# Optimization experiments

Measured on AMD Instinct MI355X. Metric: run time of the kernel, lower is better.

Reference implementation:

```python
import jax, jax.numpy as jnp
import numpy as np
import math

B, S = 2, 2048
DIM_MODEL = 2048
NUM_Q_HEADS = 16
GROUP_SIZE = 4
NUM_KV_HEADS = NUM_Q_HEADS // GROUP_SIZE
DIM_K = 128
RMS_EPS = 1e-6
ROPE_BASE = 10000.0


def setup_inputs() -> dict:
    key = jax.random.key(0)
    ks = jax.random.split(key, 8)
    x = jax.random.normal(ks[0], (B, S, DIM_MODEL), dtype=jnp.float32)
    mask = jnp.tril(jnp.ones((S, S), dtype=bool))  # causal
    # Linear weights stored as [in, out] so y = x @ W (bias=False everywhere)
    sd = 1.0 / math.sqrt(DIM_MODEL)
    Wq = jax.random.uniform(ks[1], (DIM_MODEL, DIM_K * NUM_Q_HEADS), jnp.float32, -sd, sd)
    Wk = jax.random.uniform(ks[2], (DIM_MODEL, DIM_K * NUM_KV_HEADS), jnp.float32, -sd, sd)
    Wv = jax.random.uniform(ks[3], (DIM_MODEL, DIM_K * NUM_KV_HEADS), jnp.float32, -sd, sd)
    sf = 1.0 / math.sqrt(DIM_K * NUM_Q_HEADS)
    Wfc = jax.random.uniform(ks[4], (DIM_K * NUM_Q_HEADS, DIM_MODEL), jnp.float32, -sf, sf)
    q_gamma = jnp.ones((DIM_K,), dtype=jnp.float32)
    k_gamma = jnp.ones((DIM_K,), dtype=jnp.float32)
    return {"x": x, "mask": mask, "Wq": Wq, "Wk": Wk, "Wv": Wv,
            "Wfc": Wfc, "q_gamma": q_gamma, "k_gamma": k_gamma}


def _rope(t):
    # t: [B, H, S, D], rotate-half RoPE
    d = t.shape[-1]
    half = d // 2
    inv_freq = 1.0 / (ROPE_BASE ** (jnp.arange(half, dtype=jnp.float32) / half))
    pos = jnp.arange(t.shape[2], dtype=jnp.float32)
    ang = pos[:, None] * inv_freq[None, :]            # [S, half]
    cos, sin = jnp.cos(ang), jnp.sin(ang)              # [S, half]
    t1, t2 = t[..., :half], t[..., half:]
    return jnp.concatenate([t1 * cos - t2 * sin, t2 * cos + t1 * sin], axis=-1)


def _rmsnorm(t, gamma):
    ms = jnp.mean(t * t, axis=-1, keepdims=True)
    return t * jax.lax.rsqrt(ms + RMS_EPS) * gamma


def reference(x, mask, Wq, Wk, Wv, Wfc, q_gamma, k_gamma):
    b, s, _ = x.shape
    q = (x @ Wq).reshape(b, s, NUM_Q_HEADS, DIM_K).transpose(0, 2, 1, 3)   # [B,Hq,S,D]
    k = (x @ Wk).reshape(b, s, NUM_KV_HEADS, DIM_K).transpose(0, 2, 1, 3)  # [B,Hkv,S,D]
    v = (x @ Wv).reshape(b, s, NUM_KV_HEADS, DIM_K).transpose(0, 2, 1, 3)
    q = _rmsnorm(_rope(q), q_gamma)
    k = _rmsnorm(_rope(k), k_gamma)
    q = q.reshape(b, NUM_KV_HEADS, GROUP_SIZE, s, DIM_K)                    # [B,Hkv,G,S,D]
    scores = jnp.einsum('bhgqd,bhkd->bhgqk', q, k) / math.sqrt(DIM_K)      # [B,Hkv,G,S,S]
    scores = jnp.where(mask, scores, -jnp.inf)
    attn = jax.nn.softmax(scores, axis=-1)  # dropout is identity in eval
    out = jnp.einsum('bhgqk,bhkd->bhgqd', attn, v)                          # [B,Hkv,G,S,D]
    out = out.reshape(b, NUM_Q_HEADS, s, DIM_K).transpose(0, 2, 1, 3)
    out = out.reshape(b, s, NUM_Q_HEADS * DIM_K) @ Wfc                      # [B,S,DM]
    return out
```

## Files before the change

kernel.cpp:

```cpp
#include <hip/hip_runtime.h>
#include <hip/hip_bf16.h>

typedef __attribute__((ext_vector_type(8))) short bf16x8;
typedef __attribute__((ext_vector_type(4))) short bf16x4;
typedef __attribute__((ext_vector_type(4))) float f32x4;

#define S_LEN 2048
#define DMODEL 2048
#define NQH 16
#define NKVH 4
#define DK 128

__device__ __forceinline__ float b2f(short u) {
  union { unsigned int i; float f; } x;
  x.i = ((unsigned int)(unsigned short)u) << 16;
  return x.f;
}
__device__ __forceinline__ short f2b(float f) {
  union { float f; unsigned int i; } x; x.f = f;
  unsigned int r = (x.i + 0x7fffu + ((x.i >> 16) & 1u)) >> 16;
  return (short)r;
}
__device__ __forceinline__ unsigned int cvtpk(float a, float b) {
  unsigned int r;
  asm("v_cvt_pk_bf16_f32 %0, %1, %2" : "=v"(r) : "v"(a), "v"(b));
  return r;
}
__device__ __forceinline__ f32x4 mfma16(bf16x8 a, bf16x8 b, f32x4 c) {
  return __builtin_amdgcn_mfma_f32_16x16x32_bf16(a, b, c, 0, 0, 0);
}
__device__ __forceinline__ void async16(short* lds, const short* g) {
  __builtin_amdgcn_global_load_lds(
      (const __attribute__((address_space(1))) unsigned int*)(const void*)g,
      (__attribute__((address_space(3))) unsigned int*)(void*)lds, 16, 0, 0);
}

__global__ void f32_to_bf16(const float* __restrict__ in, short* __restrict__ out, int n4) {
  int i = blockIdx.x * blockDim.x + threadIdx.x;
  if (i >= n4) return;
  float4 v = ((const float4*)in)[i];
  bf16x4 o;
  o[0] = f2b(v.x); o[1] = f2b(v.y); o[2] = f2b(v.z); o[3] = f2b(v.w);
  ((bf16x4*)out)[i] = o;
}

__global__ void rope_table(float* __restrict__ rt) {
  int i = blockIdx.x * blockDim.x + threadIdx.x;
  int s = i >> 6, d = i & 63;
  float ang = (float)s * __expf((float)d * -0.14391157f);
  float c, sn;
  __sincosf(ang, &sn, &c);
  rt[s * 128 + d] = c;
  rt[s * 128 + 64 + d] = sn;
}

__global__ void transpose_f2b(const float* __restrict__ in, short* __restrict__ out,
                              int R, int C) {
  __shared__ short t[32][33];
  int c0 = blockIdx.x * 32, r0 = blockIdx.y * 32;
  int tx = threadIdx.x, ty = threadIdx.y;
#pragma unroll
  for (int i = 0; i < 32; i += 8)
    t[ty + i][tx] = f2b(in[(size_t)(r0 + ty + i) * C + c0 + tx]);
  __syncthreads();
#pragma unroll
  for (int i = 0; i < 32; i += 8)
    out[(size_t)(c0 + ty + i) * R + r0 + tx] = t[tx][ty + i];
}

__device__ __forceinline__ void stage_tile64(short* Ls, const short* Gb, int ldg,
                                             int w, int lane) {
#pragma unroll
  for (int i = 0; i < 4; ++i) {
    const int r0 = w * 32 + i * 8;
    const int row = r0 + (lane >> 3);
    const int colb = ((lane & 7) * 8) ^ ((row & 7) << 3);
    async16(Ls + r0 * 64, Gb + (size_t)row * ldg + colb);
  }
}

__global__ __launch_bounds__(256) void gemm_qkv(const short* __restrict__ A,
                                                const short* __restrict__ WT,
                                                short* __restrict__ Qr,
                                                short* __restrict__ Kr,
                                                short* __restrict__ Vtr,
                                                const float* __restrict__ qg,
                                                const float* __restrict__ kg,
                                                const float* __restrict__ ropeT) {
  constexpr int CS_LD = 136;
  __shared__ __align__(16) short smem[4 * 128 * 64];

  const int flat = blockIdx.x;
  const int xcd = flat & 7, idx = flat >> 3;
  const int mb = (xcd >> 1) * 8 + (idx & 7);
  const int nb = (xcd & 1) * 12 + (idx >> 3);

  const int tid = threadIdx.x;
  const int lane = tid & 63;
  const int w = tid >> 6;
  const int wm = w >> 1, wn = w & 1;
  const int l15 = lane & 15, lg = lane >> 4;
  const int K = DMODEL;
  constexpr int NSTEP = DMODEL / 64;

  f32x4 acc[4][4] = {};
  const short* Ab = A + (size_t)mb * 128 * K;
  const short* Bb = WT + (size_t)nb * 128 * K;

  stage_tile64(smem, Ab, K, w, lane);
  stage_tile64(smem + 8192, Bb, K, w, lane);
  asm volatile("s_waitcnt vmcnt(0)" ::: "memory");
  __syncthreads();

  for (int t = 0; t < NSTEP; ++t) {
    const int cur = t & 1;
    short* Ac = smem + cur * 16384;
    short* Bc = Ac + 8192;
    if (t + 1 < NSTEP) {
      short* An = smem + (cur ^ 1) * 16384;
      stage_tile64(An, Ab + (t + 1) * 64, K, w, lane);
      stage_tile64(An + 8192, Bb + (t + 1) * 64, K, w, lane);
    }
#pragma unroll
    for (int kk = 0; kk < 2; ++kk) {
      bf16x8 af[4], bfr[4];
#pragma unroll
      for (int mt = 0; mt < 4; ++mt)
        af[mt] = *(const bf16x8*)(Ac + (wm * 64 + mt * 16 + l15) * 64 +
                                  ((kk * 32 + lg * 8) ^ ((l15 & 7) << 3)));
#pragma unroll
      for (int nt = 0; nt < 4; ++nt)
        bfr[nt] = *(const bf16x8*)(Bc + (wn * 64 + nt * 16 + l15) * 64 +
                                   ((kk * 32 + lg * 8) ^ ((l15 & 7) << 3)));
#pragma unroll
      for (int mt = 0; mt < 4; ++mt)
#pragma unroll
        for (int nt = 0; nt < 4; ++nt)
          acc[mt][nt] = mfma16(af[mt], bfr[nt], acc[mt][nt]);
    }
    asm volatile("s_waitcnt vmcnt(0)" ::: "memory");
    __syncthreads();
  }

  short* Cs = smem;
#pragma unroll
  for (int mt = 0; mt < 4; ++mt)
#pragma unroll
    for (int nt = 0; nt < 4; ++nt)
#pragma unroll
      for (int r = 0; r < 4; ++r)
        Cs[(wm * 64 + mt * 16 + lg * 4 + r) * CS_LD + wn * 64 + nt * 16 + l15] =
            f2b(acc[mt][nt][r]);
  __syncthreads();

  const int srow0 = mb * 128;
  const int b = srow0 >> 11;

  if (nb < 20) {
    const bool isQ = nb < 16;
    const int h = isQ ? nb : nb - 16;
    const float* gamma = isQ ? qg : kg;
    const int r = tid >> 1, half = tid & 1;
    const int s = (srow0 + r) & 2047;
    const float* rt = ropeT + (size_t)s * 128;
    float ss = 0.f;
    bf16x8 ov[8];
#pragma unroll
    for (int j = 0; j < 8; ++j) {
      bf16x8 t1v = *(const bf16x8*)(Cs + r * CS_LD + j * 8);
      bf16x8 t2v = *(const bf16x8*)(Cs + r * CS_LD + 64 + j * 8);
      float4 c0 = *(const float4*)(rt + j * 8);
      float4 c1 = *(const float4*)(rt + j * 8 + 4);
      float4 s0 = *(const float4*)(rt + 64 + j * 8);
      float4 s1 = *(const float4*)(rt + 64 + j * 8 + 4);
      float cc[8] = {c0.x, c0.y, c0.z, c0.w, c1.x, c1.y, c1.z, c1.w};
      float sn[8] = {s0.x, s0.y, s0.z, s0.w, s1.x, s1.y, s1.z, s1.w};
#pragma unroll
      for (int i = 0; i < 8; ++i) {
        float t1 = b2f(t1v[i]), t2 = b2f(t2v[i]);
        float o = half ? (t2 * cc[i] + t1 * sn[i]) : (t1 * cc[i] - t2 * sn[i]);
        ss += o * o;
        ov[j][i] = f2b(o);
      }
    }
    ss += __shfl_xor(ss, 1);
    float inv = rsqrtf(ss * (1.0f / 128.0f) + 1e-6f);
    if (isQ) inv *= (0.08838834764831845f * 1.4426950408889634f);
    const int NH = isQ ? NQH : NKVH;
    short* outp = isQ ? Qr : Kr;
    short* ob = outp + ((size_t)(b * NH + h) * S_LEN + s) * DK + half * 64;
#pragma unroll
    for (int j = 0; j < 8; ++j) {
      float4 g0 = *(const float4*)(gamma + half * 64 + j * 8);
      float4 g1 = *(const float4*)(gamma + half * 64 + j * 8 + 4);
      float gg[8] = {g0.x, g0.y, g0.z, g0.w, g1.x, g1.y, g1.z, g1.w};
      bf16x8 vv;
#pragma unroll
      for (int i = 0; i < 8; ++i) vv[i] = f2b(b2f(ov[j][i]) * inv * gg[i]);
      *(bf16x8*)(ob + j * 8) = vv;
    }
  } else {
    const int h = nb - 20;
    const int d = tid & 127;
    const int sh = tid >> 7;
    const int sbase = (srow0 & 2047) + sh * 64;
    short* ob = Vtr + ((size_t)(b * NKVH + h) * DK + d) * S_LEN + sbase;
    for (int i0 = 0; i0 < 64; i0 += 8) {
      bf16x8 v;
#pragma unroll
      for (int j = 0; j < 8; ++j) {
        const int p = i0 + j;
        const int sl = sh * 64 + 16 * (p & 3) + (p >> 2);
        v[j] = Cs[sl * CS_LD + d];
      }
      *(bf16x8*)(ob + i0) = v;
    }
  }
}

__global__ __launch_bounds__(256) void gemm_out(const short* __restrict__ A,
                                                const short* __restrict__ BT,
                                                float* __restrict__ outf) {
  __shared__ __align__(16) short smem[4 * 128 * 64];

  const int flat = blockIdx.x;
  const int xcd = flat & 7, idx = flat >> 3;
  const int mb = (xcd >> 1) * 8 + (idx & 7);
  const int nb = (xcd & 1) * 8 + (idx >> 3);

  const int tid = threadIdx.x;
  const int lane = tid & 63;
  const int w = tid >> 6;
  const int wm = w >> 1, wn = w & 1;
  const int l15 = lane & 15, lg = lane >> 4;
  const int K = NQH * DK, N = DMODEL;
  constexpr int NSTEP = (NQH * DK) / 64;

  f32x4 acc[4][4] = {};
  const short* Ab = A + (size_t)mb * 128 * K;
  const short* Bb = BT + (size_t)nb * 128 * K;

  stage_tile64(smem, Ab, K, w, lane);
  stage_tile64(smem + 8192, Bb, K, w, lane);
  asm volatile("s_waitcnt vmcnt(0)" ::: "memory");
  __syncthreads();

  for (int t = 0; t < NSTEP; ++t) {
    const int cur = t & 1;
    short* Ac = smem + cur * 16384;
    short* Bc = Ac + 8192;
    if (t + 1 < NSTEP) {
      short* An = smem + (cur ^ 1) * 16384;
      stage_tile64(An, Ab + (t + 1) * 64, K, w, lane);
      stage_tile64(An + 8192, Bb + (t + 1) * 64, K, w, lane);
    }
#pragma unroll
    for (int kk = 0; kk < 2; ++kk) {
      bf16x8 af[4], bfr[4];
#pragma unroll
      for (int mt = 0; mt < 4; ++mt)
        af[mt] = *(const bf16x8*)(Ac + (wm * 64 + mt * 16 + l15) * 64 +
                                  ((kk * 32 + lg * 8) ^ ((l15 & 7) << 3)));
#pragma unroll
      for (int nt = 0; nt < 4; ++nt)
        bfr[nt] = *(const bf16x8*)(Bc + (wn * 64 + nt * 16 + l15) * 64 +
                                   ((kk * 32 + lg * 8) ^ ((l15 & 7) << 3)));
#pragma unroll
      for (int mt = 0; mt < 4; ++mt)
#pragma unroll
        for (int nt = 0; nt < 4; ++nt)
          acc[mt][nt] = mfma16(af[mt], bfr[nt], acc[mt][nt]);
    }
    asm volatile("s_waitcnt vmcnt(0)" ::: "memory");
    __syncthreads();
  }

#pragma unroll
  for (int mt = 0; mt < 4; ++mt) {
    const int row = mb * 128 + wm * 64 + mt * 16 + lg * 4;
#pragma unroll
    for (int nt = 0; nt < 4; ++nt) {
      const int col = nb * 128 + wn * 64 + nt * 16 + l15;
#pragma unroll
      for (int r = 0; r < 4; ++r)
        outf[(size_t)(row + r) * N + col] = acc[mt][nt][r];
    }
  }
}

__device__ __forceinline__ void stage_kv(const short* __restrict__ Kb,
                                         const short* __restrict__ Vb, int kb,
                                         short* Ks, short* Vs, int w, int lane) {
#pragma unroll
  for (int i = 0; i < 4; ++i) {
    const int c = 4 * w + i;
    const int krow = c * 4 + (lane >> 4);
    const int kcol = (((lane & 15) * 16) ^ ((krow & 7) << 4)) >> 1;
    async16(Ks + c * 512, Kb + (size_t)(kb + krow) * DK + kcol);
    const int vrow = c * 8 + (lane >> 3);
    const int vcol = (((lane & 7) * 16) ^ ((vrow & 7) << 4)) >> 1;
    async16(Vs + c * 512, Vb + (size_t)vrow * S_LEN + kb + vcol);
  }
}

__device__ __forceinline__ void sm_pv(f32x4* sc, float* lsum, f32x4* acco,
                                      const short* Vc, short* Pw, int q0, bool diag,
                                      int kb, int l15, int lg) {
  if (diag) {
#pragma unroll
    for (int nt = 0; nt < 4; ++nt) {
      const int k = kb + nt * 16 + l15;
#pragma unroll
      for (int r = 0; r < 4; ++r)
        if (k > q0 + lg * 4 + r) sc[nt][r] = -1e30f;
    }
  }
#pragma unroll
  for (int r = 0; r < 4; ++r) {
    const float p0 = exp2f(sc[0][r]);
    const float p1 = exp2f(sc[1][r]);
    const float p2 = exp2f(sc[2][r]);
    const float p3 = exp2f(sc[3][r]);
    lsum[r] += (p0 + p1) + (p2 + p3);
    uint2 dv;
    dv.x = cvtpk(p0, p1);
    dv.y = cvtpk(p2, p3);
    *(uint2*)(Pw + (lg * 4 + r) * 72 + l15 * 4) = dv;
  }
#pragma unroll
  for (int kk = 0; kk < 2; ++kk) {
    bf16x8 ap = *(const bf16x8*)(Pw + l15 * 72 + kk * 32 + lg * 8);
#pragma unroll
    for (int dt = 0; dt < 8; ++dt) {
      const int vrow = dt * 16 + l15;
      bf16x8 bv = *(const bf16x8*)(Vc + vrow * 64 +
                                   (((kk * 64 + lg * 16) ^ ((vrow & 7) << 4)) >> 1));
      acco[dt] = mfma16(ap, bv, acco[dt]);
    }
  }
}

__device__ __forceinline__ void attn_writeout(f32x4* acco, float* lsum,
                                              short* __restrict__ AO, int b, int qh,
                                              int q0, int l15, int lg) {
  float ls[4];
#pragma unroll
  for (int r = 0; r < 4; ++r) {
    float t = lsum[r];
    t += __shfl_xor(t, 1);
    t += __shfl_xor(t, 2);
    t += __shfl_xor(t, 4);
    t += __shfl_xor(t, 8);
    ls[r] = 1.0f / t;
  }
  short* ob = AO + (size_t)(b * S_LEN + q0) * (NQH * DK) + qh * DK;
#pragma unroll
  for (int dt = 0; dt < 8; ++dt)
#pragma unroll
    for (int r = 0; r < 4; ++r)
      ob[(size_t)(lg * 4 + r) * (NQH * DK) + dt * 16 + l15] = f2b(acco[dt][r] * ls[r]);
}

__global__ __launch_bounds__(256, 2) void attn_kernel(const short* __restrict__ Qr,
                                                      const short* __restrict__ Kr,
                                                      const short* __restrict__ Vt,
                                                      short* __restrict__ AO) {
  const int flat = blockIdx.x;
  const int nw = (flat & 7) * 64 + (flat >> 3);
  const int qtA = nw & 15;
  const int bh = nw >> 4;
  const int qtB = 31 - qtA;
  const int b = bh >> 4, qh = bh & 15;
  const int kvh = qh >> 2;
  const short* Qb = Qr + (size_t)bh * S_LEN * DK;
  const short* Kb = Kr + (size_t)(b * NKVH + kvh) * S_LEN * DK;
  const short* Vb = Vt + (size_t)(b * NKVH + kvh) * DK * S_LEN;
  const int tid = threadIdx.x, lane = tid & 63, w = tid >> 6;
  const int l15 = lane & 15, lg = lane >> 4;

  __shared__ __align__(16) short KV[4][64 * 128];
  __shared__ __align__(16) short P[4][16][72];
  short* Pw = &P[w][0][0];

  const int q0A = qtA * 64 + w * 16, q0B = qtB * 64 + w * 16;
  bf16x8 aqA[4], aqB[4];
#pragma unroll
  for (int kk = 0; kk < 4; ++kk) {
    aqA[kk] = *(const bf16x8*)(Qb + (size_t)(q0A + l15) * DK + kk * 32 + lg * 8);
    aqB[kk] = *(const bf16x8*)(Qb + (size_t)(q0B + l15) * DK + kk * 32 + lg * 8);
  }

  f32x4 accoA[8] = {}, accoB[8] = {};
  float lsA[4] = {0.f, 0.f, 0.f, 0.f}, lsB[4] = {0.f, 0.f, 0.f, 0.f};

  short* Kcur = KV[0]; short* Vcur = KV[1];
  short* Knxt = KV[2]; short* Vnxt = KV[3];

  stage_kv(Kb, Vb, 0, Kcur, Vcur, w, lane);
  asm volatile("s_waitcnt vmcnt(0)" ::: "memory");
  __syncthreads();

  for (int kt = 0; kt <= qtB; ++kt) {
    const int kb = kt * 64;
    if (kt < qtB) stage_kv(Kb, Vb, kb + 64, Knxt, Vnxt, w, lane);

    if (kt <= qtA) {
      f32x4 scB[4] = {}, scA[4] = {};
#pragma unroll
      for (int kk = 0; kk < 4; ++kk)
#pragma unroll
        for (int nt = 0; nt < 4; ++nt) {
          const int krow = nt * 16 + l15;
          bf16x8 bk = *(const bf16x8*)(Kcur + krow * 128 +
                                       (((kk * 64 + lg * 16) ^ ((krow & 7) << 4)) >> 1));
          scB[nt] = mfma16(aqB[kk], bk, scB[nt]);
          scA[nt] = mfma16(aqA[kk], bk, scA[nt]);
        }
      sm_pv(scB, lsB, accoB, Vcur, Pw, q0B, false, kb, l15, lg);
      sm_pv(scA, lsA, accoA, Vcur, Pw, q0A, kt == qtA, kb, l15, lg);
    } else {
      f32x4 scB[4] = {};
#pragma unroll
      for (int kk = 0; kk < 4; ++kk)
#pragma unroll
        for (int nt = 0; nt < 4; ++nt) {
          const int krow = nt * 16 + l15;
          bf16x8 bk = *(const bf16x8*)(Kcur + krow * 128 +
                                       (((kk * 64 + lg * 16) ^ ((krow & 7) << 4)) >> 1));
          scB[nt] = mfma16(aqB[kk], bk, scB[nt]);
        }
      sm_pv(scB, lsB, accoB, Vcur, Pw, q0B, kt == qtB, kb, l15, lg);
    }

    asm volatile("s_waitcnt vmcnt(0)" ::: "memory");
    __syncthreads();
    short* t;
    t = Kcur; Kcur = Knxt; Knxt = t;
    t = Vcur; Vcur = Vnxt; Vnxt = t;
  }

  attn_writeout(accoB, lsB, AO, b, qh, q0B, l15, lg);
  attn_writeout(accoA, lsA, AO, b, qh, q0A, l15, lg);
}

extern "C" void kernel_launch(void* const* d_in, const int* in_sizes, int n_in,
                              void* d_out, int out_size, void* d_ws, size_t ws_size,
                              hipStream_t stream) {
  const float* x = (const float*)d_in[0];
  const float* Wq = (const float*)d_in[2];
  const float* Wk = (const float*)d_in[3];
  const float* Wv = (const float*)d_in[4];
  const float* Wfc = (const float*)d_in[5];
  const float* qg = (const float*)d_in[6];
  const float* kg = (const float*)d_in[7];

  short* ws = (short*)d_ws;
  short* xb = ws;
  short* WqkvT = xb + (size_t)4096 * 2048;
  short* WqT = WqkvT;
  short* WkT = WqT + (size_t)2048 * 2048;
  short* WvT = WkT + (size_t)512 * 2048;
  short* WfcT = WvT + (size_t)512 * 2048;
  short* Qr = WfcT + (size_t)2048 * 2048;
  short* Kr = Qr + (size_t)32 * 2048 * 128;
  short* Vt = Kr + (size_t)8 * 2048 * 128;
  float* ropeT = (float*)(Vt + (size_t)8 * 128 * 2048);
  short* AO = xb;

  f32_to_bf16<<<(4096 * 2048 / 4 + 255) / 256, 256, 0, stream>>>(x, xb, 4096 * 2048 / 4);
  rope_table<<<(2048 * 64 + 255) / 256, 256, 0, stream>>>(ropeT);

  dim3 tb(32, 8);
  transpose_f2b<<<dim3(2048 / 32, 2048 / 32), tb, 0, stream>>>(Wq, WqT, 2048, 2048);
  transpose_f2b<<<dim3(512 / 32, 2048 / 32), tb, 0, stream>>>(Wk, WkT, 2048, 512);
  transpose_f2b<<<dim3(512 / 32, 2048 / 32), tb, 0, stream>>>(Wv, WvT, 2048, 512);
  transpose_f2b<<<dim3(2048 / 32, 2048 / 32), tb, 0, stream>>>(Wfc, WfcT, 2048, 2048);

  gemm_qkv<<<768, 256, 0, stream>>>(xb, WqkvT, Qr, Kr, Vt, qg, kg, ropeT);

  attn_kernel<<<512, 256, 0, stream>>>(Qr, Kr, Vt, AO);

  gemm_out<<<512, 256, 0, stream>>>(AO, WfcT, (float*)d_out);
}
```

Baseline: 198.1 us.

## Restructure GEMM mainloop into half-K-step staging with partial vmcnt waits

Replaces the double-buffered 64-wide K-step loop in both projection GEMMs with a shared core. It stages 32-wide K halves into separate LDS slices using a new XOR swizzle, and waits with vmcnt(4) so one half-tile load stays in flight while the other is consumed. The full vmcnt(0) drain per step goes away, and plain s_barrier replaces __syncthreads. This trades more barriers per K-step for finer-grained overlap, and hardcodes K=2048 for both kernels.

```diff
diff --git a/kernel.cpp b/kernel.cpp
--- a/kernel.cpp
+++ b/kernel.cpp
@@ -68,15 +68,89 @@
     out[(size_t)(c0 + ty + i) * R + r0 + tx] = t[tx][ty + i];
 }
 
-__device__ __forceinline__ void stage_tile64(short* Ls, const short* Gb, int ldg,
-                                             int w, int lane) {
-#pragma unroll
-  for (int i = 0; i < 4; ++i) {
-    const int r0 = w * 32 + i * 8;
-    const int row = r0 + (lane >> 3);
-    const int colb = ((lane & 7) * 8) ^ ((row & 7) << 3);
-    async16(Ls + r0 * 64, Gb + (size_t)row * ldg + colb);
-  }
+__device__ __forceinline__ void kcore128(const short* __restrict__ Ab,
+                                         const short* __restrict__ Bb,
+                                         short* sm, f32x4 (&acc)[4][4],
+                                         int w, int lane, int wm, int wn,
+                                         int l15, int lg) {
+  const int K = 2048;
+  const int srow = 32 * w + (lane >> 2);
+  const int colp = (((lane & 3) ^ ((srow >> 1) & 3)) * 8);
+  const short* pA0 = Ab + (size_t)srow * K + colp;
+  const short* pA1 = pA0 + (size_t)16 * K;
+  const short* pB0 = Bb + (size_t)srow * K + colp;
+  const short* pB1 = pB0 + (size_t)16 * K;
+  const int sdst = w * 1024;
+  const int perm = (l15 >> 1) & 3;
+  const int aoff = (wm * 64 + l15) * 32 + ((lg ^ perm) * 8);
+  const int boff = 8192 + (wn * 64 + l15) * 32 + ((lg ^ perm) * 8);
+
+  auto stage = [&](int bufn, int tn, int h) {
+    short* d = sm + bufn * 16384 + h * 4096 + sdst;
+    const int off = tn * 64 + h * 32;
+    async16(d, pA0 + off);
+    async16(d + 512, pA1 + off);
+    async16(d + 8192, pB0 + off);
+    async16(d + 8192 + 512, pB1 + off);
+  };
+  auto half = [&](int bc, int h) {
+    const short* base = sm + bc * 16384 + h * 4096;
+    bf16x8 af[4], bfr[4];
+#pragma unroll
+    for (int mt = 0; mt < 4; ++mt) af[mt] = *(const bf16x8*)(base + aoff + mt * 512);
+#pragma unroll
+    for (int nt = 0; nt < 4; ++nt) bfr[nt] = *(const bf16x8*)(base + boff + nt * 512);
+#pragma unroll
+    for (int mt = 0; mt < 4; ++mt)
+#pragma unroll
+      for (int nt = 0; nt < 4; ++nt)
+        acc[mt][nt] = mfma16(af[mt], bfr[nt], acc[mt][nt]);
+  };
+
+  stage(0, 0, 0);
+  stage(0, 0, 1);
+
+#pragma unroll 1
+  for (int tt = 0; tt < 30; tt += 2) {
+    asm volatile("s_waitcnt vmcnt(4)" ::: "memory");
+    __builtin_amdgcn_s_barrier();
+    asm volatile("" ::: "memory");
+    stage(1, tt + 1, 0);
+    half(0, 0);
+    asm volatile("s_waitcnt vmcnt(4)" ::: "memory");
+    __builtin_amdgcn_s_barrier();
+    asm volatile("" ::: "memory");
+    stage(1, tt + 1, 1);
+    half(0, 1);
+    asm volatile("s_waitcnt vmcnt(4)" ::: "memory");
+    __builtin_amdgcn_s_barrier();
+    asm volatile("" ::: "memory");
+    stage(0, tt + 2, 0);
+    half(1, 0);
+    asm volatile("s_waitcnt vmcnt(4)" ::: "memory");
+    __builtin_amdgcn_s_barrier();
+    asm volatile("" ::: "memory");
+    stage(0, tt + 2, 1);
+    half(1, 1);
+  }
+  asm volatile("s_waitcnt vmcnt(4)" ::: "memory");
+  __builtin_amdgcn_s_barrier();
+  asm volatile("" ::: "memory");
+  stage(1, 31, 0);
+  half(0, 0);
+  asm volatile("s_waitcnt vmcnt(4)" ::: "memory");
+  __builtin_amdgcn_s_barrier();
+  asm volatile("" ::: "memory");
+  stage(1, 31, 1);
+  half(0, 1);
+  asm volatile("s_waitcnt vmcnt(4)" ::: "memory");
+  __builtin_amdgcn_s_barrier();
+  asm volatile("" ::: "memory");
+  half(1, 0);
+  asm volatile("s_waitcnt vmcnt(0)" ::: "memory");
+  __builtin_amdgcn_s_barrier();
+  asm volatile("" ::: "memory");
+  half(1, 1);
 }
 
 __global__ __launch_bounds__(256) void gemm_qkv(const short* __restrict__ A,
@@ -88,7 +162,7 @@
                                                 const float* __restrict__ kg,
                                                 const float* __restrict__ ropeT) {
   constexpr int CS_LD = 136;
-  __shared__ __align__(16) short smem[4 * 128 * 64];
+  __shared__ __align__(16) short smem[32768];
 
   const int flat = blockIdx.x;
   const int xcd = flat & 7, idx = flat >> 3;
@@ -101,47 +175,12 @@
   const int wm = w >> 1, wn = w & 1;
   const int l15 = lane & 15, lg = lane >> 4;
   const int K = DMODEL;
-  constexpr int NSTEP = DMODEL / 64;
 
   f32x4 acc[4][4] = {};
-  const short* Ab = A + (size_t)mb * 128 * K;
-  const short* Bb = WT + (size_t)nb * 128 * K;
-
-  stage_tile64(smem, Ab, K, w, lane);
-  stage_tile64(smem + 8192, Bb, K, w, lane);
-  asm volatile("s_waitcnt vmcnt(0)" ::: "memory");
+  kcore128(A + (size_t)mb * 128 * K, WT + (size_t)nb * 128 * K, smem, acc,
+           w, lane, wm, wn, l15, lg);
+
   __syncthreads();
-
-  for (int t = 0; t < NSTEP; ++t) {
-    const int cur = t & 1;
-    short* Ac = smem + cur * 16384;
-    short* Bc = Ac + 8192;
-    if (t + 1 < NSTEP) {
-      short* An = smem + (cur ^ 1) * 16384;
-      stage_tile64(An, Ab + (t + 1) * 64, K, w, lane);
-      stage_tile64(An + 8192, Bb + (t + 1) * 64, K, w, lane);
-    }
-#pragma unroll
-    for (int kk = 0; kk < 2; ++kk) {
-      bf16x8 af[4], bfr[4];
-#pragma unroll
-      for (int mt = 0; mt < 4; ++mt)
-        af[mt] = *(const bf16x8*)(Ac + (wm * 64 + mt * 16 + l15) * 64 +
-                                  ((kk * 32 + lg * 8) ^ ((l15 & 7) << 3)));
-#pragma unroll
-      for (int nt = 0; nt < 4; ++nt)
-        bfr[nt] = *(const bf16x8*)(Bc + (wn * 64 + nt * 16 + l15) * 64 +
-                                   ((kk * 32 + lg * 8) ^ ((l15 & 7) << 3)));
-#pragma unroll
-      for (int mt = 0; mt < 4; ++mt)
-#pragma unroll
-        for (int nt = 0; nt < 4; ++nt)
-          acc[mt][nt] = mfma16(af[mt], bfr[nt], acc[mt][nt]);
-    }
-    asm volatile("s_waitcnt vmcnt(0)" ::: "memory");
-    __syncthreads();
-  }
-
   short* Cs = smem;
 #pragma unroll
   for (int mt = 0; mt < 4; ++mt)
@@ -221,7 +260,7 @@
 __global__ __launch_bounds__(256) void gemm_out(const short* __restrict__ A,
                                                 const short* __restrict__ BT,
                                                 float* __restrict__ outf) {
-  __shared__ __align__(16) short smem[4 * 128 * 64];
+  __shared__ __align__(16) short smem[32768];
 
   const int flat = blockIdx.x;
   const int xcd = flat & 7, idx = flat >> 3;
@@ -234,46 +273,10 @@
   const int wm = w >> 1, wn = w & 1;
   const int l15 = lane & 15, lg = lane >> 4;
   const int K = NQH * DK, N = DMODEL;
-  constexpr int NSTEP = (NQH * DK) / 64;
 
   f32x4 acc[4][4] = {};
-  const short* Ab = A + (size_t)mb * 128 * K;
-  const short* Bb = BT + (size_t)nb * 128 * K;
-
-  stage_tile64(smem, Ab, K, w, lane);
-  stage_tile64(smem + 8192, Bb, K, w, lane);
-  asm volatile("s_waitcnt vmcnt(0)" ::: "memory");
-  __syncthreads();
-
-  for (int t = 0; t < NSTEP; ++t) {
-    const int cur = t & 1;
-    short* Ac = smem + cur * 16384;
-    short* Bc = Ac + 8192;
-    if (t + 1 < NSTEP) {
-      short* An = smem + (cur ^ 1) * 16384;
-      stage_tile64(An, Ab + (t + 1) * 64, K, w, lane);
-      stage_tile64(An + 8192, Bb + (t + 1) * 64, K, w, lane);
-    }
-#pragma unroll
-    for (int kk = 0; kk < 2; ++kk) {
-      bf16x8 af[4], bfr[4];
-#pragma unroll
-      for (int mt = 0; mt < 4; ++mt)
-        af[mt] = *(const bf16x8*)(Ac + (wm * 64 + mt * 16 + l15) * 64 +
-                                  ((kk * 32 + lg * 8) ^ ((l15 & 7) << 3)));
-#pragma unroll
-      for (int nt = 0; nt < 4; ++nt)
-        bfr[nt] = *(const bf16x8*)(Bc + (wn * 64 + nt * 16 + l15) * 64 +
-                                   ((kk * 32 + lg * 8) ^ ((l15 & 7) << 3)));
-#pragma unroll
-      for (int mt = 0; mt < 4; ++mt)
-#pragma unroll
-        for (int nt = 0; nt < 4; ++nt)
-          acc[mt][nt] = mfma16(af[mt], bfr[nt], acc[mt][nt]);
-    }
-    asm volatile("s_waitcnt vmcnt(0)" ::: "memory");
-    __syncthreads();
-  }
+  kcore128(A + (size_t)mb * 128 * K, BT + (size_t)nb * 128 * K, smem, acc,
+           w, lane, wm, wn, l15, lg);
 
 #pragma unroll
   for (int mt = 0; mt < 4; ++mt) {
```

After: 199.3 us. About the same (+0.6%).

## Rewrite QKV and output GEMMs with 256-row tiles and triple-buffered pipeline

Applied to the files above, without the earlier changes.

Both projection GEMMs move to a shared 512-thread core with 256x256 (QKV) and 256x128 (out) block tiles, a K-step of 32 and three LDS buffers. Loads are issued asynchronously, interleaved with MFMA, and raised with s_setprio so global traffic overlaps compute. The QKV epilogue now runs in two 128-row phases covering two heads per tile. Bigger tiles raise arithmetic intensity and cut block count, but 192 or 256 blocks may leave parts of the 256 CUs idle, and register pressure rises.

```diff
diff --git a/kernel.cpp b/kernel.cpp
--- a/kernel.cpp
+++ b/kernel.cpp
@@ -68,18 +68,102 @@
     out[(size_t)(c0 + ty + i) * R + r0 + tx] = t[tx][ty + i];
 }
 
-__device__ __forceinline__ void stage_tile64(short* Ls, const short* Gb, int ldg,
-                                             int w, int lane) {
-#pragma unroll
-  for (int i = 0; i < 4; ++i) {
-    const int r0 = w * 32 + i * 8;
-    const int row = r0 + (lane >> 3);
-    const int colb = ((lane & 7) * 8) ^ ((row & 7) << 3);
-    async16(Ls + r0 * 64, Gb + (size_t)row * ldg + colb);
-  }
-}
-
-__global__ __launch_bounds__(256) void gemm_qkv(const short* __restrict__ A,
+template <int NT, int VW>
+__device__ __forceinline__ void kcore256(const short* __restrict__ Ab,
+                                         const short* __restrict__ Bb,
+                                         short* sm, f32x4 (&acc)[8][NT], int tid) {
+  const int K = 2048;
+  const int lane = tid & 63, w = tid >> 6;
+  const int wm2 = w >> 2, wn4 = w & 3;
+  const int l15 = lane & 15, lg = lane >> 4;
+  constexpr int ABUF = 8192;
+  constexpr int BBUF = NT * 2048;
+  constexpr int BUFSZ = ABUF + BBUF;
+
+  const int sr = lane >> 2, sc = lane & 3;
+  const int ar0 = w * 16 + sr, ar1 = ar0 + 128;
+  const short* gA0 = Ab + (size_t)ar0 * K + ((sc ^ (ar0 & 3)) * 8);
+  const short* gA1 = Ab + (size_t)ar1 * K + ((sc ^ (ar1 & 3)) * 8);
+  const short* gB0 = Bb + (size_t)ar0 * K + ((sc ^ (ar0 & 3)) * 8);
+  const short* gB1 = Bb + (size_t)ar1 * K + ((sc ^ (ar1 & 3)) * 8);
+  const int dA0 = (w * 16) * 32, dA1 = dA0 + 128 * 32;
+  const int dB0 = ABUF + dA0, dB1 = ABUF + dA1;
+
+  int aoff[8], boff[NT];
+#pragma unroll
+  for (int mt = 0; mt < 8; ++mt) {
+    const int row = wm2 * 128 + mt * 16 + l15;
+    aoff[mt] = row * 32 + ((lg * 8) ^ ((row & 3) << 3));
+  }
+#pragma unroll
+  for (int nt = 0; nt < NT; ++nt) {
+    const int row = wn4 * (NT * 16) + nt * 16 + l15;
+    boff[nt] = ABUF + row * 32 + ((lg * 8) ^ ((row & 3) << 3));
+  }
+
+  auto stageA = [&](int buf, int t) {
+    short* d = sm + buf * BUFSZ;
+    const int o = t * 32;
+    async16(d + dA0, gA0 + o);
+    async16(d + dA1, gA1 + o);
+  };
+  auto stageB = [&](int buf, int t) {
+    short* d = sm + buf * BUFSZ;
+    const int o = t * 32;
+    async16(d + dB0, gB0 + o);
+    if constexpr (NT == 4) async16(d + dB1, gB1 + o);
+  };
+  auto tilebody = [&](int buf, int sbuf, int st, bool dostage) {
+    const short* bc = sm + buf * BUFSZ;
+    if (dostage) stageA(sbuf, st);
+    bf16x8 bfr[NT], af[4];
+#pragma unroll
+    for (int nt = 0; nt < NT; ++nt) bfr[nt] = *(const bf16x8*)(bc + boff[nt]);
+#pragma unroll
+    for (int mt = 0; mt < 4; ++mt) af[mt] = *(const bf16x8*)(bc + aoff[mt]);
+    __builtin_amdgcn_s_setprio(1);
+#pragma unroll
+    for (int mt = 0; mt < 4; ++mt)
+#pragma unroll
+      for (int nt = 0; nt < NT; ++nt)
+        acc[mt][nt] = mfma16(af[mt], bfr[nt], acc[mt][nt]);
+    __builtin_amdgcn_s_setprio(0);
+    if (dostage) stageB(sbuf, st);
+#pragma unroll
+    for (int mt = 0; mt < 4; ++mt) af[mt] = *(const bf16x8*)(bc + aoff[4 + mt]);
+    __builtin_amdgcn_s_setprio(1);
+#pragma unroll
+    for (int mt = 0; mt < 4; ++mt)
+#pragma unroll
+      for (int nt = 0; nt < NT; ++nt)
+        acc[4 + mt][nt] = mfma16(af[mt], bfr[nt], acc[4 + mt][nt]);
+    __builtin_amdgcn_s_setprio(0);
+  };
+
+  stageA(0, 0); stageB(0, 0);
+  stageA(1, 1); stageB(1, 1);
+  int cur = 0, nx2 = 2;
+#pragma unroll 1
+  for (int t = 0; t < 63; ++t) {
+    __builtin_amdgcn_sched_barrier(0);
+    if constexpr (VW == 4)
+      asm volatile("s_waitcnt vmcnt(4)" ::: "memory");
+    else
+      asm volatile("s_waitcnt vmcnt(3)" ::: "memory");
+    __builtin_amdgcn_s_barrier();
+    __builtin_amdgcn_sched_barrier(0);
+    tilebody(cur, nx2, t + 2, t < 62);
+    cur = (cur == 2) ? 0 : cur + 1;
+    nx2 = (nx2 == 2) ? 0 : nx2 + 1;
+  }
+  __builtin_amdgcn_sched_barrier(0);
+  asm volatile("s_waitcnt vmcnt(0)" ::: "memory");
+  __builtin_amdgcn_s_barrier();
+  __builtin_amdgcn_sched_barrier(0);
+  tilebody(cur, 0, 0, false);
+}
+
+__global__ __launch_bounds__(512) void gemm_qkv(const short* __restrict__ A,
                                                 const short* __restrict__ WT,
                                                 short* __restrict__ Qr,
                                                 short* __restrict__ Kr,
@@ -87,203 +171,129 @@
                                                 const float* __restrict__ qg,
                                                 const float* __restrict__ kg,
                                                 const float* __restrict__ ropeT) {
-  constexpr int CS_LD = 136;
-  __shared__ __align__(16) short smem[4 * 128 * 64];
-
+  __shared__ __align__(16) short smem[49152];
   const int flat = blockIdx.x;
   const int xcd = flat & 7, idx = flat >> 3;
-  const int mb = (xcd >> 1) * 8 + (idx & 7);
-  const int nb = (xcd & 1) * 12 + (idx >> 3);
-
+  const int mb = (xcd >> 1) * 4 + (idx & 3);
+  const int nb = (xcd & 1) * 6 + (idx >> 2);
   const int tid = threadIdx.x;
-  const int lane = tid & 63;
-  const int w = tid >> 6;
-  const int wm = w >> 1, wn = w & 1;
+
+  f32x4 acc[8][4] = {};
+  kcore256<4, 4>(A + (size_t)mb * 256 * 2048, WT + (size_t)nb * 256 * 2048,
+                 smem, acc, tid);
+
+  const int lane = tid & 63, w = tid >> 6, wm2 = w >> 2, wn4 = w & 3;
   const int l15 = lane & 15, lg = lane >> 4;
-  const int K = DMODEL;
-  constexpr int NSTEP = DMODEL / 64;
-
-  f32x4 acc[4][4] = {};
-  const short* Ab = A + (size_t)mb * 128 * K;
-  const short* Bb = WT + (size_t)nb * 128 * K;
-
-  stage_tile64(smem, Ab, K, w, lane);
-  stage_tile64(smem + 8192, Bb, K, w, lane);
-  asm volatile("s_waitcnt vmcnt(0)" ::: "memory");
-  __syncthreads();
-
-  for (int t = 0; t < NSTEP; ++t) {
-    const int cur = t & 1;
-    short* Ac = smem + cur * 16384;
-    short* Bc = Ac + 8192;
-    if (t + 1 < NSTEP) {
-      short* An = smem + (cur ^ 1) * 16384;
-      stage_tile64(An, Ab + (t + 1) * 64, K, w, lane);
-      stage_tile64(An + 8192, Bb + (t + 1) * 64, K, w, lane);
-    }
-#pragma unroll
-    for (int kk = 0; kk < 2; ++kk) {
-      bf16x8 af[4], bfr[4];
-#pragma unroll
-      for (int mt = 0; mt < 4; ++mt)
-        af[mt] = *(const bf16x8*)(Ac + (wm * 64 + mt * 16 + l15) * 64 +
-                                  ((kk * 32 + lg * 8) ^ ((l15 & 7) << 3)));
-#pragma unroll
-      for (int nt = 0; nt < 4; ++nt)
-        bfr[nt] = *(const bf16x8*)(Bc + (wn * 64 + nt * 16 + l15) * 64 +
-                                   ((kk * 32 + lg * 8) ^ ((l15 & 7) << 3)));
-#pragma unroll
-      for (int mt = 0; mt < 4; ++mt)
+  const int b = mb >> 3;
+  short* Cs = smem;
+  constexpr int CL = 264;
+
+  for (int ph = 0; ph < 2; ++ph) {
+    __syncthreads();
+    if (wm2 == ph) {
+#pragma unroll
+      for (int mt = 0; mt < 8; ++mt)
 #pragma unroll
         for (int nt = 0; nt < 4; ++nt)
-          acc[mt][nt] = mfma16(af[mt], bfr[nt], acc[mt][nt]);
-    }
-    asm volatile("s_waitcnt vmcnt(0)" ::: "memory");
+#pragma unroll
+          for (int rr = 0; rr < 4; ++rr)
+            Cs[(mt * 16 + lg * 4 + rr) * CL + wn4 * 64 + nt * 16 + l15] =
+                f2b(acc[mt][nt][rr]);
+    }
     __syncthreads();
-  }
-
-  short* Cs = smem;
-#pragma unroll
-  for (int mt = 0; mt < 4; ++mt)
-#pragma unroll
-    for (int nt = 0; nt < 4; ++nt)
-#pragma unroll
-      for (int r = 0; r < 4; ++r)
-        Cs[(wm * 64 + mt * 16 + lg * 4 + r) * CS_LD + wn * 64 + nt * 16 + l15] =
-            f2b(acc[mt][nt][r]);
-  __syncthreads();
-
-  const int srow0 = mb * 128;
-  const int b = srow0 >> 11;
-
-  if (nb < 20) {
-    const bool isQ = nb < 16;
-    const int h = isQ ? nb : nb - 16;
-    const float* gamma = isQ ? qg : kg;
-    const int r = tid >> 1, half = tid & 1;
-    const int s = (srow0 + r) & 2047;
-    const float* rt = ropeT + (size_t)s * 128;
-    float ss = 0.f;
-    bf16x8 ov[8];
-#pragma unroll
-    for (int j = 0; j < 8; ++j) {
-      bf16x8 t1v = *(const bf16x8*)(Cs + r * CS_LD + j * 8);
-      bf16x8 t2v = *(const bf16x8*)(Cs + r * CS_LD + 64 + j * 8);
-      float4 c0 = *(const float4*)(rt + j * 8);
-      float4 c1 = *(const float4*)(rt + j * 8 + 4);
-      float4 s0 = *(const float4*)(rt + 64 + j * 8);
-      float4 s1 = *(const float4*)(rt + 64 + j * 8 + 4);
-      float cc[8] = {c0.x, c0.y, c0.z, c0.w, c1.x, c1.y, c1.z, c1.w};
-      float sn[8] = {s0.x, s0.y, s0.z, s0.w, s1.x, s1.y, s1.z, s1.w};
-#pragma unroll
-      for (int i = 0; i < 8; ++i) {
-        float t1 = b2f(t1v[i]), t2 = b2f(t2v[i]);
-        float o = half ? (t2 * cc[i] + t1 * sn[i]) : (t1 * cc[i] - t2 * sn[i]);
-        ss += o * o;
-        ov[j][i] = f2b(o);
+    const int srowg = mb * 256 + ph * 128;
+    if (nb < 10) {
+      const bool isQ = nb < 8;
+      const int r = tid >> 2, quad = tid & 3;
+      const int head = quad >> 1, half = quad & 1;
+      const int s = (srowg + r) & 2047;
+      const float* rt = ropeT + (size_t)s * 128;
+      const short* crow = Cs + r * CL + head * 128;
+      const float* gamma = isQ ? qg : kg;
+      float ss = 0.f;
+      bf16x8 ov[8];
+#pragma unroll
+      for (int j = 0; j < 8; ++j) {
+        bf16x8 t1v = *(const bf16x8*)(crow + j * 8);
+        bf16x8 t2v = *(const bf16x8*)(crow + 64 + j * 8);
+        float4 c0 = *(const float4*)(rt + j * 8);
+        float4 c1 = *(const float4*)(rt + j * 8 + 4);
+        float4 s0 = *(const float4*)(rt + 64 + j * 8);
+        float4 s1 = *(const float4*)(rt + 64 + j * 8 + 4);
+        float cc[8] = {c0.x, c0.y, c0.z, c0.w, c1.x, c1.y, c1.z, c1.w};
+        float sn[8] = {s0.x, s0.y, s0.z, s0.w, s1.x, s1.y, s1.z, s1.w};
+#pragma unroll
+        for (int i = 0; i < 8; ++i) {
+          float t1 = b2f(t1v[i]), t2 = b2f(t2v[i]);
+          float o = half ? (t2 * cc[i] + t1 * sn[i]) : (t1 * cc[i] - t2 * sn[i]);
+          ss += o * o;
+          ov[j][i] = f2b(o);
+        }
       }
-    }
-    ss += __shfl_xor(ss, 1);
-    float inv = rsqrtf(ss * (1.0f / 128.0f) + 1e-6f);
-    if (isQ) inv *= (0.08838834764831845f * 1.4426950408889634f);
-    const int NH = isQ ? NQH : NKVH;
-    short* outp = isQ ? Qr : Kr;
-    short* ob = outp + ((size_t)(b * NH + h) * S_LEN + s) * DK + half * 64;
-#pragma unroll
-    for (int j = 0; j < 8; ++j) {
-      float4 g0 = *(const float4*)(gamma + half * 64 + j * 8);
-      float4 g1 = *(const float4*)(gamma + half * 64 + j * 8 + 4);
-      float gg[8] = {g0.x, g0.y, g0.z, g0.w, g1.x, g1.y, g1.z, g1.w};
-      bf16x8 vv;
-#pragma unroll
-      for (int i = 0; i < 8; ++i) vv[i] = f2b(b2f(ov[j][i]) * inv * gg[i]);
-      *(bf16x8*)(ob + j * 8) = vv;
-    }
-  } else {
-    const int h = nb - 20;
-    const int d = tid & 127;
-    const int sh = tid >> 7;
-    const int sbase = (srow0 & 2047) + sh * 64;
-    short* ob = Vtr + ((size_t)(b * NKVH + h) * DK + d) * S_LEN + sbase;
-    for (int i0 = 0; i0 < 64; i0 += 8) {
-      bf16x8 v;
+      ss += __shfl_xor(ss, 1);
+      float inv = rsqrtf(ss * (1.0f / 128.0f) + 1e-6f);
+      if (isQ) inv *= (0.08838834764831845f * 1.4426950408889634f);
+      const int NH = isQ ? NQH : NKVH;
+      const int hg = isQ ? (nb * 2 + head) : ((nb - 8) * 2 + head);
+      short* outp = isQ ? Qr : Kr;
+      short* ob = outp + ((size_t)(b * NH + hg) * S_LEN + s) * DK + half * 64;
 #pragma unroll
       for (int j = 0; j < 8; ++j) {
-        const int p = i0 + j;
-        const int sl = sh * 64 + 16 * (p & 3) + (p >> 2);
-        v[j] = Cs[sl * CS_LD + d];
+        float4 g0 = *(const float4*)(gamma + half * 64 + j * 8);
+        float4 g1 = *(const float4*)(gamma + half * 64 + j * 8 + 4);
+        float gg[8] = {g0.x, g0.y, g0.z, g0.w, g1.x, g1.y, g1.z, g1.w};
+        bf16x8 vv;
+#pragma unroll
+        for (int i = 0; i < 8; ++i) vv[i] = f2b(b2f(ov[j][i]) * inv * gg[i]);
+        *(bf16x8*)(ob + j * 8) = vv;
       }
-      *(bf16x8*)(ob + i0) = v;
-    }
-  }
-}
-
-__global__ __launch_bounds__(256) void gemm_out(const short* __restrict__ A,
+    } else {
+      const int hd = tid >> 7;
+      const int head = hd >> 1, sh = hd & 1;
+      const int d = tid & 127;
+      const int hg = (nb - 10) * 2 + head;
+      const int sbase = (srowg & 2047) + sh * 64;
+      short* ob = Vtr + ((size_t)(b * NKVH + hg) * DK + d) * S_LEN + sbase;
+      const short* cc = Cs + head * 128 + d;
+      for (int i0 = 0; i0 < 64; i0 += 8) {
+        bf16x8 v;
+#pragma unroll
+        for (int j = 0; j < 8; ++j) {
+          const int p = i0 + j;
+          const int sl = sh * 64 + 16 * (p & 3) + (p >> 2);
+          v[j] = cc[sl * CL];
+        }
+        *(bf16x8*)(ob + i0) = v;
+      }
+    }
+  }
+}
+
+__global__ __launch_bounds__(512) void gemm_out(const short* __restrict__ A,
                                                 const short* __restrict__ BT,
                                                 float* __restrict__ outf) {
-  __shared__ __align__(16) short smem[4 * 128 * 64];
-
+  __shared__ __align__(16) short smem[36864];
   const int flat = blockIdx.x;
   const int xcd = flat & 7, idx = flat >> 3;
-  const int mb = (xcd >> 1) * 8 + (idx & 7);
-  const int nb = (xcd & 1) * 8 + (idx >> 3);
-
+  const int mb = (xcd >> 1) * 4 + (idx & 3);
+  const int nb = (xcd & 1) * 8 + (idx >> 2);
   const int tid = threadIdx.x;
-  const int lane = tid & 63;
-  const int w = tid >> 6;
-  const int wm = w >> 1, wn = w & 1;
+
+  f32x4 acc[8][2] = {};
+  kcore256<2, 3>(A + (size_t)mb * 256 * 2048, BT + (size_t)nb * 128 * 2048,
+                 smem, acc, tid);
+
+  const int lane = tid & 63, w = tid >> 6, wm2 = w >> 2, wn4 = w & 3;
   const int l15 = lane & 15, lg = lane >> 4;
-  const int K = NQH * DK, N = DMODEL;
-  constexpr int NSTEP = (NQH * DK) / 64;
-
-  f32x4 acc[4][4] = {};
-  const short* Ab = A + (size_t)mb * 128 * K;
-  const short* Bb = BT + (size_t)nb * 128 * K;
-
-  stage_tile64(smem, Ab, K, w, lane);
-  stage_tile64(smem + 8192, Bb, K, w, lane);
-  asm volatile("s_waitcnt vmcnt(0)" ::: "memory");
-  __syncthreads();
-
-  for (int t = 0; t < NSTEP; ++t) {
-    const int cur = t & 1;
-    short* Ac = smem + cur * 16384;
-    short* Bc = Ac + 8192;
-    if (t + 1 < NSTEP) {
-      short* An = smem + (cur ^ 1) * 16384;
-      stage_tile64(An, Ab + (t + 1) * 64, K, w, lane);
-      stage_tile64(An + 8192, Bb + (t + 1) * 64, K, w, lane);
-    }
-#pragma unroll
-    for (int kk = 0; kk < 2; ++kk) {
-      bf16x8 af[4], bfr[4];
-#pragma unroll
-      for (int mt = 0; mt < 4; ++mt)
-        af[mt] = *(const bf16x8*)(Ac + (wm * 64 + mt * 16 + l15) * 64 +
-                                  ((kk * 32 + lg * 8) ^ ((l15 & 7) << 3)));
-#pragma unroll
-      for (int nt = 0; nt < 4; ++nt)
-        bfr[nt] = *(const bf16x8*)(Bc + (wn * 64 + nt * 16 + l15) * 64 +
-                                   ((kk * 32 + lg * 8) ^ ((l15 & 7) << 3)));
-#pragma unroll
-      for (int mt = 0; mt < 4; ++mt)
-#pragma unroll
-        for (int nt = 0; nt < 4; ++nt)
-          acc[mt][nt] = mfma16(af[mt], bfr[nt], acc[mt][nt]);
-    }
-    asm volatile("s_waitcnt vmcnt(0)" ::: "memory");
-    __syncthreads();
-  }
-
-#pragma unroll
-  for (int mt = 0; mt < 4; ++mt) {
-    const int row = mb * 128 + wm * 64 + mt * 16 + lg * 4;
-#pragma unroll
-    for (int nt = 0; nt < 4; ++nt) {
-      const int col = nb * 128 + wn * 64 + nt * 16 + l15;
+#pragma unroll
+  for (int mt = 0; mt < 8; ++mt) {
+    const int row = mb * 256 + wm2 * 128 + mt * 16 + lg * 4;
+#pragma unroll
+    for (int nt = 0; nt < 2; ++nt) {
+      const int col = nb * 128 + wn4 * 32 + nt * 16 + l15;
 #pragma unroll
       for (int r = 0; r < 4; ++r)
-        outf[(size_t)(row + r) * N + col] = acc[mt][nt][r];
+        outf[(size_t)(row + r) * DMODEL + col] = acc[mt][nt][r];
     }
   }
 }
@@ -476,9 +486,9 @@
   transpose_f2b<<<dim3(512 / 32, 2048 / 32), tb, 0, stream>>>(Wv, WvT, 2048, 512);
   transpose_f2b<<<dim3(2048 / 32, 2048 / 32), tb, 0, stream>>>(Wfc, WfcT, 2048, 2048);
 
-  gemm_qkv<<<768, 256, 0, stream>>>(xb, WqkvT, Qr, Kr, Vt, qg, kg, ropeT);
+  gemm_qkv<<<192, 512, 0, stream>>>(xb, WqkvT, Qr, Kr, Vt, qg, kg, ropeT);
 
   attn_kernel<<<512, 256, 0, stream>>>(Qr, Kr, Vt, AO);
 
-  gemm_out<<<512, 256, 0, stream>>>(AO, WfcT, (float*)d_out);
-}
+  gemm_out<<<256, 512, 0, stream>>>(AO, WfcT, (float*)d_out);
+}
```

Result: slower. 216.9 us (+9.5%).
